# Kernel tuning notes

Hardware: AMD Instinct MI355X
Metric: run time of the kernel (lower is better)

Reference implementation:

```python
import jax, jax.numpy as jnp
import numpy as np
import math

H, B, T = 4, 32, 1000
EPROJS, DUNITS, DK, DV = 1024, 1024, 512, 512
ACONV_CHANS, ACONV_FILTS = 100, 100
FILTS = [ACONV_FILTS * (h + 1) // H for h in range(H)]  # 25, 50, 75, 100


def setup_inputs() -> dict:
    key = jax.random.key(0)
    ks = jax.random.split(key, 16)
    s = 0.02  # small init to keep tanh unsaturated
    ap = jax.random.uniform(ks[3], (H, B, T), dtype=jnp.float32)
    ap = ap / ap.sum(-1, keepdims=True)  # previous attention weights (rows sum to 1)
    inp = {
        "enc_hs_pad": jax.random.normal(ks[0], (B, T, EPROJS), dtype=jnp.float32),
        "enc_hs_len": jnp.full((B,), T, dtype=jnp.int32),
        "dec_z": jax.random.normal(ks[1], (B, DUNITS), dtype=jnp.float32),
        "att_prev": ap,
        "Wq": jax.random.normal(ks[4], (H, DUNITS, DK), dtype=jnp.float32) * s,
        "bq": jnp.zeros((H, DK), dtype=jnp.float32),
        "Wk": jax.random.normal(ks[5], (H, EPROJS, DK), dtype=jnp.float32) * s,
        "Wv": jax.random.normal(ks[6], (H, EPROJS, DV), dtype=jnp.float32) * s,
        "g_w": jax.random.normal(ks[7], (H, DK), dtype=jnp.float32) * s,
        "g_b": jnp.zeros((H,), dtype=jnp.float32),
        "Watt": jax.random.normal(ks[8], (H, ACONV_CHANS, DK), dtype=jnp.float32) * s,
        "Wo": jax.random.normal(ks[9], (H * DV, EPROJS), dtype=jnp.float32) * s,
    }
    for h in range(H):
        inp[f"conv_w{h}"] = jax.random.normal(ks[10 + h], (ACONV_CHANS, 1, 2 * FILTS[h] + 1), dtype=jnp.float32) * s
    return inp


def _conv1d(x, w, f):
    # x: [B, T], w: [C, 1, K]; SAME padding like torch Conv2d(padding=(0, f)) -> [B, C, T]
    return jax.lax.conv_general_dilated(x[:, None, :], w, (1,), [(f, f)],
                                        dimension_numbers=("NCH", "OIH", "NCH"))


def reference(enc_hs_pad, enc_hs_len, dec_z, att_prev, Wq, bq, Wk, Wv, g_w, g_b,
              Watt, Wo, conv_w0, conv_w1, conv_w2, conv_w3):
    scaling = 1.0 / math.sqrt(DK)
    conv_ws = [conv_w0, conv_w1, conv_w2, conv_w3]
    # per-head K/V projections of encoder states: [H, B, T, dk/dv]
    k = jnp.einsum('btd,hde->hbte', enc_hs_pad, Wk)
    v = jnp.einsum('btd,hde->hbte', enc_hs_pad, Wv)
    # per-head query projection: [H, B, dk]
    q = jnp.einsum('bd,hde->hbe', dec_z, Wq) + bq[:, None, :]
    # location features: per-head conv (different filter widths) then linear -> [H, B, T, dk]
    att_conv = jnp.stack([_conv1d(att_prev[h], conv_ws[h], FILTS[h]).transpose(0, 2, 1)
                          for h in range(H)])  # [H, B, T, C]
    att_conv = jnp.einsum('hbtc,hce->hbte', att_conv, Watt)
    # energies via gvec: [H, B, T]
    e = jnp.einsum('hbte,he->hbt', jnp.tanh(k + att_conv + q[:, :, None, :]), g_w) + g_b[:, None, None]
    w = jax.nn.softmax(scaling * e, axis=-1)  # no length masking, as in the original
    # weighted sums per head, concatenated head-major: [B, H*dv]
    c = jnp.einsum('hbte,hbt->bhe', v, w).reshape(B, H * DV)
    out = c @ Wo  # [B, eprojs]
    return out, w
```

## Files before the change

### kernel.cpp

```cpp
#include <hip/hip_runtime.h>
#include <hip/hip_bf16.h>
#include <math.h>

#define Hh 4
#define Bb 32
#define Tt 1000
#define TP 1024
#define EPROJS_ 1024
#define DUNITS_ 1024
#define DKd 512
#define DVd 512
#define CC 100
#define KPAD 256
#define SCALING 0.04419417382415922f

typedef __attribute__((ext_vector_type(8))) short short8;
typedef __attribute__((ext_vector_type(4))) float floatx4;

__device__ __forceinline__ void async16(const void* g, void* l) {
    __builtin_amdgcn_global_load_lds(
        (const __attribute__((address_space(1))) unsigned int*)g,
        (__attribute__((address_space(3))) unsigned int*)l, 16, 0, 0);
}

__device__ __forceinline__ float fast_tanh(float x) {
    float xc = fminf(fmaxf(x, -10.f), 10.f);
    float t = __expf(2.f * xc);
    return (t - 1.f) * __builtin_amdgcn_rcpf(t + 1.f);
}

__global__ __launch_bounds__(256) void enc_cvt_kernel(
    const float* __restrict__ enc, unsigned short* __restrict__ enc16)
{
    int t = blockIdx.x, b = blockIdx.y;
    int d = threadIdx.x * 4;
    float4 v = *(const float4*)(enc + ((size_t)(b * Tt + t)) * EPROJS_ + d);
    union { __hip_bfloat162 h2[2]; uint2 u; } u;
    u.h2[0] = __float22bfloat162_rn(make_float2(v.x, v.y));
    u.h2[1] = __float22bfloat162_rn(make_float2(v.z, v.w));
    *(uint2*)(enc16 + ((size_t)(b * TP + t)) * EPROJS_ + d) = u.u;
}

__global__ __launch_bounds__(256) void wkt_kernel(
    const float* __restrict__ Wk, unsigned short* __restrict__ Wkt)
{
    int et = blockIdx.x;
    int dt = blockIdx.y;
    int h  = blockIdx.z;
    __shared__ float tile[64][65];
    int tid = threadIdx.x;
    int r = tid >> 4, c4 = tid & 15;
    const float* src = Wk + ((size_t)(h * DUNITS_ + dt * 64)) * DKd + et * 64;
#pragma unroll
    for (int rr = 0; rr < 4; ++rr) {
        int row = r + rr * 16;
        *(float4*)&tile[row][c4 * 4] = *(const float4*)(src + (size_t)row * DKd + c4 * 4);
    }
    __syncthreads();
    unsigned short* dst = Wkt + ((size_t)(h * DKd + et * 64)) * EPROJS_ + dt * 64;
#pragma unroll
    for (int rr = 0; rr < 4; ++rr) {
        int el = r + rr * 16;
        union { __hip_bfloat162 h2[2]; uint2 u; } u;
        u.h2[0] = __float22bfloat162_rn(make_float2(tile[c4 * 4 + 0][el], tile[c4 * 4 + 1][el]));
        u.h2[1] = __float22bfloat162_rn(make_float2(tile[c4 * 4 + 2][el], tile[c4 * 4 + 3][el]));
        *(uint2*)(dst + (size_t)el * EPROJS_ + c4 * 4) = u.u;
    }
}

__global__ __launch_bounds__(256) void ww_kernel(
    const float* __restrict__ w0, const float* __restrict__ w1,
    const float* __restrict__ w2, const float* __restrict__ w3,
    const float* __restrict__ Watt, __hip_bfloat16* __restrict__ WWt)
{
    int k = blockIdx.x;
    int h = blockIdx.y;
    int f = 25 * (h + 1), Kh = 2 * f + 1;
    const float* cw = (h == 0) ? w0 : (h == 1) ? w1 : (h == 2) ? w2 : w3;
    int e = threadIdx.x;
    float acc0 = 0.f, acc1 = 0.f;
    if (k < Kh) {
        for (int c = 0; c < CC; ++c) {
            float wv = cw[c * Kh + k];
            acc0 += wv * Watt[(h * CC + c) * DKd + e];
            acc1 += wv * Watt[(h * CC + c) * DKd + e + 256];
        }
    }
    WWt[((size_t)(h * DKd + e)) * KPAD + k] = __float2bfloat16(acc0);
    WWt[((size_t)(h * DKd + e + 256)) * KPAD + k] = __float2bfloat16(acc1);
}

__global__ __launch_bounds__(256) void q_kernel(
    const float* __restrict__ dec_z, const float* __restrict__ Wq,
    float* __restrict__ q_buf)
{
    int et = blockIdx.x, kc = blockIdx.y, h = blockIdx.z;
    int d0 = kc * 64;
    __shared__ float zs[32][64];
    int tid = threadIdx.x;
    {
        int b = tid >> 3, dc = (tid & 7) * 8;
        const float* p = dec_z + (size_t)b * DUNITS_ + d0 + dc;
        *(float4*)&zs[b][dc] = *(const float4*)p;
        *(float4*)&zs[b][dc + 4] = *(const float4*)(p + 4);
    }
    __syncthreads();
    int e = et * 128 + (tid & 127);
    int dl0 = (tid >> 7) * 32;
    float wq[32];
#pragma unroll
    for (int dl = 0; dl < 32; ++dl)
        wq[dl] = Wq[((size_t)(h * DUNITS_ + d0 + dl0 + dl)) * DKd + e];
#pragma unroll
    for (int b = 0; b < 32; ++b) {
        float s = 0.f;
#pragma unroll
        for (int dl = 0; dl < 32; ++dl) s += zs[b][dl0 + dl] * wq[dl];
        atomicAdd(&q_buf[(h * Bb + b) * DKd + e], s);
    }
}

__global__ __launch_bounds__(256) void e_kernel(
    const unsigned short* __restrict__ enc16, const unsigned short* __restrict__ Wkt,
    const float* __restrict__ att_prev, const __hip_bfloat16* __restrict__ WWt,
    const float* __restrict__ q_buf, const float* __restrict__ bq,
    const float* __restrict__ g_w, float* __restrict__ e_buf)
{
    const int lin = blockIdx.x;
    const int xcd = lin & 7, pos = lin >> 3;
    const int b = (pos >> 7) * 8 + xcd;
    const int rem = pos & 127;
    const int h = rem >> 5;
    const int by = (rem & 31) >> 2;
    const int bx = rem & 3;
    const int t0 = by * 128, e0 = bx * 128;
    const int tid = threadIdx.x;
    const int lane = tid & 63, w = tid >> 6;
    const int wr = w >> 1, wc = w & 1;
    const int m = lane & 15, quad = lane >> 4;
    const int srow = tid >> 3;
    const int ko = (((tid & 7) ^ (srow & 7))) * 8;
    const int sw = m & 7;

    __shared__ __align__(16) short As[2][128 * 64];
    __shared__ __align__(16) short Bs[2][128 * 64];

    floatx4 acc[4][4];
#pragma unroll
    for (int i = 0; i < 4; ++i)
#pragma unroll
        for (int j = 0; j < 4; ++j) acc[i][j] = (floatx4){0.f, 0.f, 0.f, 0.f};

    const unsigned short* WkB = Wkt + ((size_t)(h * DKd + e0)) * EPROJS_;
    const unsigned short* encB = enc16 + ((size_t)(b * TP + t0)) * EPROJS_;

    auto stage1 = [&](int chunk, int bi) {
        const int d0 = chunk * 64;
        char* ad = (char*)As[bi] + (tid & ~63) * 16;
        char* bd = (char*)Bs[bi] + (tid & ~63) * 16;
#pragma unroll
        for (int it = 0; it < 4; ++it) {
            int r2 = it * 32 + srow;
            async16(encB + (size_t)r2 * EPROJS_ + d0 + ko, ad + it * 4096);
            async16(WkB + (size_t)r2 * EPROJS_ + d0 + ko, bd + it * 4096);
        }
    };

    stage1(0, 0);
    for (int ch = 0; ch < 16; ++ch) {
        const int cur = ch & 1;
        if (ch < 15) {
            stage1(ch + 1, cur ^ 1);
            asm volatile("s_waitcnt vmcnt(8)" ::: "memory");
        } else {
            asm volatile("s_waitcnt vmcnt(0)" ::: "memory");
        }
        __builtin_amdgcn_sched_barrier(0);
        __builtin_amdgcn_s_barrier();
        __builtin_amdgcn_sched_barrier(0);
#pragma unroll
        for (int ks = 0; ks < 2; ++ks) {
            short8 af[4], bf[4];
#pragma unroll
            for (int i = 0; i < 4; ++i)
                af[i] = *(const short8*)&As[cur][(wr * 64 + i * 16 + m) * 64 + (((ks << 2) + quad) ^ sw) * 8];
#pragma unroll
            for (int j = 0; j < 4; ++j)
                bf[j] = *(const short8*)&Bs[cur][(wc * 64 + j * 16 + m) * 64 + (((ks << 2) + quad) ^ sw) * 8];
#pragma unroll
            for (int i = 0; i < 4; ++i)
#pragma unroll
                for (int j = 0; j < 4; ++j)
                    acc[i][j] = __builtin_amdgcn_mfma_f32_16x16x32_bf16(
                        af[i], bf[j], acc[i][j], 0, 0, 0);
        }
        __builtin_amdgcn_sched_barrier(0);
        __builtin_amdgcn_s_barrier();
        __builtin_amdgcn_sched_barrier(0);
    }

    const int f = 25 * (h + 1);
    const int Kh = 2 * f + 1;
    const int nch2 = (Kh + 63) >> 6;
    const float* ab = att_prev + (size_t)(h * Bb + b) * Tt;
    const __hip_bfloat16* WWB = WWt + ((size_t)(h * DKd + e0)) * KPAD;
    char* BsDst0 = (char*)Bs[0] + (tid & ~63) * 16;
    for (int ch = 0; ch < nch2; ++ch) {
        int k0 = ch * 64;
        int ar = tid >> 1, half = tid & 1;
        int sbase = t0 + ar - f + k0 + half * 32;
        float v[32];
#pragma unroll
        for (int j2 = 0; j2 < 32; ++j2) {
            int s = sbase + j2;
            v[j2] = (s >= 0 && s < Tt) ? ab[s] : 0.f;
        }
        __syncthreads();
#pragma unroll
        for (int it = 0; it < 4; ++it) {
            int r2 = it * 32 + srow;
            async16(WWB + (size_t)r2 * KPAD + k0 + ko, BsDst0 + it * 4096);
        }
        union { short8 s[4]; __hip_bfloat162 hh[16]; } u;
#pragma unroll
        for (int j2 = 0; j2 < 16; ++j2)
            u.hh[j2] = __float22bfloat162_rn(make_float2(v[2 * j2], v[2 * j2 + 1]));
#pragma unroll
        for (int jj = 0; jj < 4; ++jj) {
            int phys = (half * 4 + jj) ^ (ar & 7);
            *(short8*)&As[0][ar * 64 + phys * 8] = u.s[jj];
        }
        __syncthreads();
#pragma unroll
        for (int ks = 0; ks < 2; ++ks) {
            short8 af[4], bf[4];
#pragma unroll
            for (int i = 0; i < 4; ++i)
                af[i] = *(const short8*)&As[0][(wr * 64 + i * 16 + m) * 64 + (((ks << 2) + quad) ^ sw) * 8];
#pragma unroll
            for (int j = 0; j < 4; ++j)
                bf[j] = *(const short8*)&Bs[0][(wc * 64 + j * 16 + m) * 64 + (((ks << 2) + quad) ^ sw) * 8];
#pragma unroll
            for (int i = 0; i < 4; ++i)
#pragma unroll
                for (int j = 0; j < 4; ++j)
                    acc[i][j] = __builtin_amdgcn_mfma_f32_16x16x32_bf16(
                        af[i], bf[j], acc[i][j], 0, 0, 0);
        }
    }

    const float* qrow = q_buf + (size_t)(h * Bb + b) * DKd;
    const float* bqrow = bq + h * DKd;
    const float* gwrow = g_w + h * DKd;
    float qv[4], gw[4];
#pragma unroll
    for (int j = 0; j < 4; ++j) {
        int e = e0 + wc * 64 + j * 16 + m;
        qv[j] = qrow[e] + bqrow[e];
        gw[j] = gwrow[e];
    }
    float* erow = e_buf + (size_t)(h * Bb + b) * Tt;
#pragma unroll
    for (int i = 0; i < 4; ++i) {
#pragma unroll
        for (int reg = 0; reg < 4; ++reg) {
            float s = 0.f;
#pragma unroll
            for (int j = 0; j < 4; ++j)
                s += fast_tanh(acc[i][j][reg] + qv[j]) * gw[j];
            s += __shfl_xor(s, 1);
            s += __shfl_xor(s, 2);
            s += __shfl_xor(s, 4);
            s += __shfl_xor(s, 8);
            int t = t0 + wr * 64 + i * 16 + quad * 4 + reg;
            if (m == 0 && t < Tt)
                atomicAdd(&erow[t], s);
        }
    }
}

__global__ __launch_bounds__(256) void softmax_kernel(
    const float* __restrict__ e_buf, float* __restrict__ wout)
{
    int rowid = blockIdx.x;
    const float* x = e_buf + rowid * Tt;
    float* y = wout + rowid * Tt;
    int tid = threadIdx.x;
    float v[4];
    float mx = -1e30f;
#pragma unroll
    for (int k = 0; k < 4; ++k) {
        int t = tid + k * 256;
        v[k] = (t < Tt) ? x[t] * SCALING : -1e30f;
        mx = fmaxf(mx, v[k]);
    }
    for (int off = 32; off >= 1; off >>= 1) mx = fmaxf(mx, __shfl_xor(mx, off));
    __shared__ float sm[4];
    __shared__ float ss[4];
    int wave = tid >> 6;
    if ((tid & 63) == 0) sm[wave] = mx;
    __syncthreads();
    mx = fmaxf(fmaxf(sm[0], sm[1]), fmaxf(sm[2], sm[3]));
    float s = 0.f;
#pragma unroll
    for (int k = 0; k < 4; ++k) {
        int t = tid + k * 256;
        v[k] = (t < Tt) ? __expf(v[k] - mx) : 0.f;
        s += v[k];
    }
    for (int off = 32; off >= 1; off >>= 1) s += __shfl_xor(s, off);
    if ((tid & 63) == 0) ss[wave] = s;
    __syncthreads();
    s = ss[0] + ss[1] + ss[2] + ss[3];
    float inv = 1.0f / s;
#pragma unroll
    for (int k = 0; k < 4; ++k) {
        int t = tid + k * 256;
        if (t < Tt) y[t] = v[k] * inv;
    }
}

__global__ __launch_bounds__(256) void ctx_kernel(
    const float* __restrict__ wout, const unsigned short* __restrict__ enc16,
    float* __restrict__ ctx)
{
    int dch = blockIdx.x;
    int b = blockIdx.y;
    int tq = blockIdx.z;
    int t0 = tq * 250;
    int tid = threadIdx.x;
    __shared__ float wl[4][252];
    __shared__ float red[8 * 4 * 128];
    for (int i = tid; i < 1000; i += 256) {
        int h = i / 250, tl = i - h * 250;
        wl[h][tl] = wout[(h * Bb + b) * Tt + t0 + tl];
    }
    __syncthreads();
    int g = tid >> 5, c = tid & 31;
    int d0 = dch * 128;
    float4 a[4];
#pragma unroll
    for (int h = 0; h < 4; ++h) a[h] = make_float4(0.f, 0.f, 0.f, 0.f);
    const unsigned short* encB = enc16 + (size_t)b * TP * EPROJS_ + d0 + c * 4;
    for (int t = t0 + g; t < t0 + 250; t += 8) {
        uint2 raw = *(const uint2*)(encB + (size_t)t * EPROJS_);
        float x0 = __uint_as_float(raw.x << 16);
        float x1 = __uint_as_float(raw.x & 0xffff0000u);
        float x2 = __uint_as_float(raw.y << 16);
        float x3 = __uint_as_float(raw.y & 0xffff0000u);
#pragma unroll
        for (int h = 0; h < 4; ++h) {
            float wv = wl[h][t - t0];
            a[h].x += wv * x0; a[h].y += wv * x1;
            a[h].z += wv * x2; a[h].w += wv * x3;
        }
    }
#pragma unroll
    for (int h = 0; h < 4; ++h)
        *(float4*)&red[((g * 4 + h) << 7) + c * 4] = a[h];
    __syncthreads();
    for (int i = tid; i < 512; i += 256) {
        int h = i >> 7, dd = i & 127;
        float ssum = 0.f;
#pragma unroll
        for (int g2 = 0; g2 < 8; ++g2) ssum += red[((g2 * 4 + h) << 7) + dd];
        atomicAdd(&ctx[(h * Bb + b) * EPROJS_ + d0 + dd], ssum);
    }
}

__global__ __launch_bounds__(256) void c_kernel(
    const float* __restrict__ ctx, const float* __restrict__ Wv,
    float* __restrict__ c_buf)
{
    int et = blockIdx.x, kc = blockIdx.y, h = blockIdx.z;
    int d0 = kc * 64;
    __shared__ float zs[32][64];
    int tid = threadIdx.x;
    {
        int b = tid >> 3, dc = (tid & 7) * 8;
        const float* p = ctx + ((size_t)(h * Bb + b)) * EPROJS_ + d0 + dc;
        *(float4*)&zs[b][dc] = *(const float4*)p;
        *(float4*)&zs[b][dc + 4] = *(const float4*)(p + 4);
    }
    __syncthreads();
    int e = et * 128 + (tid & 127);
    int dl0 = (tid >> 7) * 32;
    float wv[32];
#pragma unroll
    for (int dl = 0; dl < 32; ++dl)
        wv[dl] = Wv[((size_t)(h * EPROJS_ + d0 + dl0 + dl)) * DVd + e];
#pragma unroll
    for (int b = 0; b < 32; ++b) {
        float s = 0.f;
#pragma unroll
        for (int dl = 0; dl < 32; ++dl) s += zs[b][dl0 + dl] * wv[dl];
        atomicAdd(&c_buf[(h * Bb + b) * DVd + e], s);
    }
}

__global__ __launch_bounds__(256) void out_kernel(
    const float* __restrict__ c_buf, const float* __restrict__ Wo,
    float* __restrict__ outp)
{
    int ot = blockIdx.x;
    int kc = blockIdx.y;
    int k0 = kc * 64, o0 = ot * 128;
    __shared__ float cs[32][64];
    int tid = threadIdx.x;
    {
        int b = tid >> 3, k8 = (tid & 7) * 8;
        int h = k0 >> 9;
        const float* p = c_buf + ((size_t)(h * Bb + b)) * DVd + (k0 & 511) + k8;
        *(float4*)&cs[b][k8] = *(const float4*)p;
        *(float4*)&cs[b][k8 + 4] = *(const float4*)(p + 4);
    }
    __syncthreads();
    int o = o0 + (tid & 127);
    int kl0 = (tid >> 7) * 32;
    float wo[32];
#pragma unroll
    for (int kl = 0; kl < 32; ++kl)
        wo[kl] = Wo[((size_t)(k0 + kl0 + kl)) * EPROJS_ + o];
#pragma unroll
    for (int b = 0; b < 32; ++b) {
        float s = 0.f;
#pragma unroll
        for (int kl = 0; kl < 32; ++kl) s += cs[b][kl0 + kl] * wo[kl];
        atomicAdd(&outp[b * EPROJS_ + o], s);
    }
}

extern "C" void kernel_launch(void* const* d_in, const int* in_sizes, int n_in,
                              void* d_out, int out_size, void* d_ws, size_t ws_size,
                              hipStream_t stream) {
    const float* enc     = (const float*)d_in[0];
    const float* dec_z   = (const float*)d_in[2];
    const float* att_prev= (const float*)d_in[3];
    const float* Wq      = (const float*)d_in[4];
    const float* bq      = (const float*)d_in[5];
    const float* Wk      = (const float*)d_in[6];
    const float* Wv      = (const float*)d_in[7];
    const float* g_w     = (const float*)d_in[8];
    const float* Watt    = (const float*)d_in[10];
    const float* Wo      = (const float*)d_in[11];
    const float* cw0     = (const float*)d_in[12];
    const float* cw1     = (const float*)d_in[13];
    const float* cw2     = (const float*)d_in[14];
    const float* cw3     = (const float*)d_in[15];

    float* ws    = (float*)d_ws;
    float* q_buf = ws;
    float* e_buf = ws + 65536;
    float* c_buf = ws + 193536;
    float* ctx   = ws + 259072;
    unsigned short* enc16 = (unsigned short*)(ws + 390144);
    unsigned short* Wkt   = (unsigned short*)(ws + 17167360);
    __hip_bfloat16* WWt   = (__hip_bfloat16*)(ws + 18215936);
    float* outp  = (float*)d_out;
    float* wout  = outp + 32768;

    hipMemsetAsync(ws, 0, (size_t)390144 * sizeof(float), stream);
    hipMemsetAsync(d_out, 0, (size_t)32768 * sizeof(float), stream);

    enc_cvt_kernel<<<dim3(Tt, Bb), 256, 0, stream>>>(enc, enc16);
    wkt_kernel<<<dim3(8, 16, 4), 256, 0, stream>>>(Wk, Wkt);
    ww_kernel<<<dim3(KPAD, 4), 256, 0, stream>>>(cw0, cw1, cw2, cw3, Watt, WWt);
    q_kernel<<<dim3(4, 16, 4), 256, 0, stream>>>(dec_z, Wq, q_buf);
    e_kernel<<<4096, 256, 0, stream>>>(enc16, Wkt, att_prev, WWt,
                                       q_buf, bq, g_w, e_buf);
    softmax_kernel<<<128, 256, 0, stream>>>(e_buf, wout);
    ctx_kernel<<<dim3(8, 32, 4), 256, 0, stream>>>(wout, enc16, ctx);
    c_kernel<<<dim3(4, 16, 4), 256, 0, stream>>>(ctx, Wv, c_buf);
    out_kernel<<<dim3(8, 32), 256, 0, stream>>>(c_buf, Wo, outp);
}
```

Baseline: 573.2 us.

## Enlarge energy GEMM tiles to 256x256 with 1024-thread blocks; merge prep kernels

The energy kernel now computes 256x256 output tiles per block with 16 waves (1024 threads) instead of 128x128 with 4 waves. This halves redundant global loads of encoder and Wk tiles and cuts the block count from 4096 to 1024. The staging loops, the wait counts and the location-conv tile fill are adjusted to match. Separately, the Wk transpose, conv-weight fold and query projection kernels are merged into one launch to save launch overhead. The larger tile uses 128KB of LDS for the double buffers, which allows only one block per CU, and the epilogue code not shown must also be correct for the new tile layout.

```diff
diff --git a/kernel.cpp b/kernel.cpp
--- a/kernel.cpp
+++ b/kernel.cpp
@@ -41,86 +41,82 @@
     *(uint2*)(enc16 + ((size_t)(b * TP + t)) * EPROJS_ + d) = u.u;
 }
 
-__global__ __launch_bounds__(256) void wkt_kernel(
-    const float* __restrict__ Wk, unsigned short* __restrict__ Wkt)
-{
-    int et = blockIdx.x;
-    int dt = blockIdx.y;
-    int h  = blockIdx.z;
-    __shared__ float tile[64][65];
-    int tid = threadIdx.x;
-    int r = tid >> 4, c4 = tid & 15;
-    const float* src = Wk + ((size_t)(h * DUNITS_ + dt * 64)) * DKd + et * 64;
-#pragma unroll
-    for (int rr = 0; rr < 4; ++rr) {
-        int row = r + rr * 16;
-        *(float4*)&tile[row][c4 * 4] = *(const float4*)(src + (size_t)row * DKd + c4 * 4);
-    }
-    __syncthreads();
-    unsigned short* dst = Wkt + ((size_t)(h * DKd + et * 64)) * EPROJS_ + dt * 64;
-#pragma unroll
-    for (int rr = 0; rr < 4; ++rr) {
-        int el = r + rr * 16;
-        union { __hip_bfloat162 h2[2]; uint2 u; } u;
-        u.h2[0] = __float22bfloat162_rn(make_float2(tile[c4 * 4 + 0][el], tile[c4 * 4 + 1][el]));
-        u.h2[1] = __float22bfloat162_rn(make_float2(tile[c4 * 4 + 2][el], tile[c4 * 4 + 3][el]));
-        *(uint2*)(dst + (size_t)el * EPROJS_ + c4 * 4) = u.u;
-    }
-}
-
-__global__ __launch_bounds__(256) void ww_kernel(
+__global__ __launch_bounds__(256) void prep_kernel(
+    const float* __restrict__ Wk, unsigned short* __restrict__ Wkt,
     const float* __restrict__ w0, const float* __restrict__ w1,
     const float* __restrict__ w2, const float* __restrict__ w3,
-    const float* __restrict__ Watt, __hip_bfloat16* __restrict__ WWt)
-{
-    int k = blockIdx.x;
-    int h = blockIdx.y;
-    int f = 25 * (h + 1), Kh = 2 * f + 1;
-    const float* cw = (h == 0) ? w0 : (h == 1) ? w1 : (h == 2) ? w2 : w3;
-    int e = threadIdx.x;
-    float acc0 = 0.f, acc1 = 0.f;
-    if (k < Kh) {
-        for (int c = 0; c < CC; ++c) {
-            float wv = cw[c * Kh + k];
-            acc0 += wv * Watt[(h * CC + c) * DKd + e];
-            acc1 += wv * Watt[(h * CC + c) * DKd + e + 256];
-        }
-    }
-    WWt[((size_t)(h * DKd + e)) * KPAD + k] = __float2bfloat16(acc0);
-    WWt[((size_t)(h * DKd + e + 256)) * KPAD + k] = __float2bfloat16(acc1);
-}
-
-__global__ __launch_bounds__(256) void q_kernel(
+    const float* __restrict__ Watt, __hip_bfloat16* __restrict__ WWt,
     const float* __restrict__ dec_z, const float* __restrict__ Wq,
     float* __restrict__ q_buf)
 {
-    int et = blockIdx.x, kc = blockIdx.y, h = blockIdx.z;
-    int d0 = kc * 64;
-    __shared__ float zs[32][64];
-    int tid = threadIdx.x;
-    {
-        int b = tid >> 3, dc = (tid & 7) * 8;
-        const float* p = dec_z + (size_t)b * DUNITS_ + d0 + dc;
-        *(float4*)&zs[b][dc] = *(const float4*)p;
-        *(float4*)&zs[b][dc + 4] = *(const float4*)(p + 4);
-    }
-    __syncthreads();
-    int e = et * 128 + (tid & 127);
-    int dl0 = (tid >> 7) * 32;
-    float wq[32];
-#pragma unroll
-    for (int dl = 0; dl < 32; ++dl)
-        wq[dl] = Wq[((size_t)(h * DUNITS_ + d0 + dl0 + dl)) * DKd + e];
-#pragma unroll
-    for (int b = 0; b < 32; ++b) {
-        float s = 0.f;
-#pragma unroll
-        for (int dl = 0; dl < 32; ++dl) s += zs[b][dl0 + dl] * wq[dl];
-        atomicAdd(&q_buf[(h * Bb + b) * DKd + e], s);
-    }
-}
-
-__global__ __launch_bounds__(256) void e_kernel(
+    __shared__ float shbuf[64 * 65];
+    const int bid = blockIdx.x;
+    const int tid = threadIdx.x;
+    if (bid < 512) {
+        int et = bid & 7, dt = (bid >> 3) & 15, h = bid >> 7;
+        float (*tile)[65] = (float(*)[65])shbuf;
+        int r = tid >> 4, c4 = tid & 15;
+        const float* src = Wk + ((size_t)(h * DUNITS_ + dt * 64)) * DKd + et * 64;
+#pragma unroll
+        for (int rr = 0; rr < 4; ++rr) {
+            int row = r + rr * 16;
+            *(float4*)&tile[row][c4 * 4] = *(const float4*)(src + (size_t)row * DKd + c4 * 4);
+        }
+        __syncthreads();
+        unsigned short* dst = Wkt + ((size_t)(h * DKd + et * 64)) * EPROJS_ + dt * 64;
+#pragma unroll
+        for (int rr = 0; rr < 4; ++rr) {
+            int el = r + rr * 16;
+            union { __hip_bfloat162 h2[2]; uint2 u; } u;
+            u.h2[0] = __float22bfloat162_rn(make_float2(tile[c4 * 4 + 0][el], tile[c4 * 4 + 1][el]));
+            u.h2[1] = __float22bfloat162_rn(make_float2(tile[c4 * 4 + 2][el], tile[c4 * 4 + 3][el]));
+            *(uint2*)(dst + (size_t)el * EPROJS_ + c4 * 4) = u.u;
+        }
+    } else if (bid < 1536) {
+        int b2 = bid - 512;
+        int k = b2 & 255, h = b2 >> 8;
+        int f = 25 * (h + 1), Kh = 2 * f + 1;
+        const float* cw = (h == 0) ? w0 : (h == 1) ? w1 : (h == 2) ? w2 : w3;
+        int e = tid;
+        float acc0 = 0.f, acc1 = 0.f;
+        if (k < Kh) {
+            for (int c = 0; c < CC; ++c) {
+                float wv = cw[c * Kh + k];
+                acc0 += wv * Watt[(h * CC + c) * DKd + e];
+                acc1 += wv * Watt[(h * CC + c) * DKd + e + 256];
+            }
+        }
+        WWt[((size_t)(h * DKd + e)) * KPAD + k] = __float2bfloat16(acc0);
+        WWt[((size_t)(h * DKd + e + 256)) * KPAD + k] = __float2bfloat16(acc1);
+    } else {
+        int b3 = bid - 1536;
+        int et = b3 & 3, kc = (b3 >> 2) & 15, h = b3 >> 6;
+        int d0 = kc * 64;
+        float (*zs)[64] = (float(*)[64])shbuf;
+        {
+            int b = tid >> 3, dc = (tid & 7) * 8;
+            const float* p = dec_z + (size_t)b * DUNITS_ + d0 + dc;
+            *(float4*)&zs[b][dc] = *(const float4*)p;
+            *(float4*)&zs[b][dc + 4] = *(const float4*)(p + 4);
+        }
+        __syncthreads();
+        int e = et * 128 + (tid & 127);
+        int dl0 = (tid >> 7) * 32;
+        float wq[32];
+#pragma unroll
+        for (int dl = 0; dl < 32; ++dl)
+            wq[dl] = Wq[((size_t)(h * DUNITS_ + d0 + dl0 + dl)) * DKd + e];
+#pragma unroll
+        for (int b = 0; b < 32; ++b) {
+            float s = 0.f;
+#pragma unroll
+            for (int dl = 0; dl < 32; ++dl) s += zs[b][dl0 + dl] * wq[dl];
+            atomicAdd(&q_buf[(h * Bb + b) * DKd + e], s);
+        }
+    }
+}
+
+__global__ __launch_bounds__(1024) void e_kernel(
     const unsigned short* __restrict__ enc16, const unsigned short* __restrict__ Wkt,
     const float* __restrict__ att_prev, const __hip_bfloat16* __restrict__ WWt,
     const float* __restrict__ q_buf, const float* __restrict__ bq,
@@ -128,22 +124,22 @@
 {
     const int lin = blockIdx.x;
     const int xcd = lin & 7, pos = lin >> 3;
-    const int b = (pos >> 7) * 8 + xcd;
-    const int rem = pos & 127;
-    const int h = rem >> 5;
-    const int by = (rem & 31) >> 2;
-    const int bx = rem & 3;
-    const int t0 = by * 128, e0 = bx * 128;
+    const int b = (pos >> 5) * 8 + xcd;
+    const int rem = pos & 31;
+    const int h = rem >> 3;
+    const int by = (rem >> 1) & 3;
+    const int bx = rem & 1;
+    const int t0 = by * 256, e0 = bx * 256;
     const int tid = threadIdx.x;
     const int lane = tid & 63, w = tid >> 6;
-    const int wr = w >> 1, wc = w & 1;
+    const int wr = w >> 2, wc = w & 3;
     const int m = lane & 15, quad = lane >> 4;
     const int srow = tid >> 3;
     const int ko = (((tid & 7) ^ (srow & 7))) * 8;
     const int sw = m & 7;
 
-    __shared__ __align__(16) short As[2][128 * 64];
-    __shared__ __align__(16) short Bs[2][128 * 64];
+    __shared__ __align__(16) short As[2][256 * 64];
+    __shared__ __align__(16) short Bs[2][256 * 64];
 
     floatx4 acc[4][4];
 #pragma unroll
@@ -159,10 +155,10 @@
         char* ad = (char*)As[bi] + (tid & ~63) * 16;
         char* bd = (char*)Bs[bi] + (tid & ~63) * 16;
 #pragma unroll
-        for (int it = 0; it < 4; ++it) {
-            int r2 = it * 32 + srow;
-            async16(encB + (size_t)r2 * EPROJS_ + d0 + ko, ad + it * 4096);
-            async16(WkB + (size_t)r2 * EPROJS_ + d0 + ko, bd + it * 4096);
+        for (int it = 0; it < 2; ++it) {
+            int r2 = it * 128 + srow;
+            async16(encB + (size_t)r2 * EPROJS_ + d0 + ko, ad + it * 16384);
+            async16(WkB + (size_t)r2 * EPROJS_ + d0 + ko, bd + it * 16384);
         }
     };
 
@@ -171,7 +167,7 @@
         const int cur = ch & 1;
         if (ch < 15) {
             stage1(ch + 1, cur ^ 1);
-            asm volatile("s_waitcnt vmcnt(8)" ::: "memory");
+            asm volatile("s_waitcnt vmcnt(4)" ::: "memory");
         } else {
             asm volatile("s_waitcnt vmcnt(0)" ::: "memory");
         }
@@ -207,27 +203,27 @@
     char* BsDst0 = (char*)Bs[0] + (tid & ~63) * 16;
     for (int ch = 0; ch < nch2; ++ch) {
         int k0 = ch * 64;
-        int ar = tid >> 1, half = tid & 1;
-        int sbase = t0 + ar - f + k0 + half * 32;
-        float v[32];
-#pragma unroll
-        for (int j2 = 0; j2 < 32; ++j2) {
+        int ar = tid >> 2, q4 = tid & 3;
+        int sbase = t0 + ar - f + k0 + q4 * 16;
+        float v[16];
+#pragma unroll
+        for (int j2 = 0; j2 < 16; ++j2) {
             int s = sbase + j2;
             v[j2] = (s >= 0 && s < Tt) ? ab[s] : 0.f;
         }
         __syncthreads();
 #pragma unroll
-        for (int it = 0; it < 4; ++it) {
-            int r2 = it * 32 + srow;
-            async16(WWB + (size_t)r2 * KPAD + k0 + ko, BsDst0 + it * 4096);
-        }
-        union { short8 s[4]; __hip_bfloat162 hh[16]; } u;
-#pragma unroll
-        for (int j2 = 0; j2 < 16; ++j2)
+        for (int it = 0; it < 2; ++it) {
+            int r2 = it * 128 + srow;
+            async16(WWB + (size_t)r2 * KPAD + k0 + ko, BsDst0 + it * 16384);
+        }
+        union { short8 s[2]; __hip_bfloat162 hh[8]; } u;
+#pragma unroll
+        for (int j2 = 0; j2 < 8; ++j2)
             u.hh[j2] = __float22bfloat162_rn(make_float2(v[2 * j2], v[2 * j2 + 1]));
 #pragma unroll
-        for (int jj = 0; jj < 4; ++jj) {
-            int phys = (half * 4 + jj) ^ (ar & 7);
+        for (int jj = 0; jj < 2; ++jj) {
+            int phys = (q4 * 2 + jj) ^ (ar & 7);
             *(short8*)&As[0][ar * 64 + phys * 8] = u.s[jj];
         }
         __syncthreads();
@@ -463,11 +459,10 @@
     hipMemsetAsync(d_out, 0, (size_t)32768 * sizeof(float), stream);
 
     enc_cvt_kernel<<<dim3(Tt, Bb), 256, 0, stream>>>(enc, enc16);
-    wkt_kernel<<<dim3(8, 16, 4), 256, 0, stream>>>(Wk, Wkt);
-    ww_kernel<<<dim3(KPAD, 4), 256, 0, stream>>>(cw0, cw1, cw2, cw3, Watt, WWt);
-    q_kernel<<<dim3(4, 16, 4), 256, 0, stream>>>(dec_z, Wq, q_buf);
-    e_kernel<<<4096, 256, 0, stream>>>(enc16, Wkt, att_prev, WWt,
-                                       q_buf, bq, g_w, e_buf);
+    prep_kernel<<<1792, 256, 0, stream>>>(Wk, Wkt, cw0, cw1, cw2, cw3, Watt, WWt,
+                                          dec_z, Wq, q_buf);
+    e_kernel<<<1024, 1024, 0, stream>>>(enc16, Wkt, att_prev, WWt,
+                                        q_buf, bq, g_w, e_buf);
     softmax_kernel<<<128, 256, 0, stream>>>(e_buf, wout);
     ctx_kernel<<<dim3(8, 32, 4), 256, 0, stream>>>(wout, enc16, ctx);
     c_kernel<<<dim3(4, 16, 4), 256, 0, stream>>>(ctx, Wv, c_buf);
```

After: 478.8 us. -16.5%, faster.
